# Performance work log

Hardware: AMD Instinct MI355X
Metric: run time of the kernel (lower is better)

## Reference

```python
import jax, jax.numpy as jnp
import numpy as np

H = 16  # n_heads


def setup_inputs() -> dict:
    key = jax.random.key(0)
    ks = jax.random.split(key, 8)
    N, L, dm = 4, 2048, 1024
    scale = 0.02
    rn = lambda k, shape: jax.random.normal(k, shape, dtype=jnp.float32)
    return {
        "queries": rn(ks[0], (N, L, dm)),
        "keys": rn(ks[1], (N, L, dm)),
        "values": rn(ks[2], (N, L, dm)),
        "Wq": rn(ks[3], (dm, dm)) * scale, "bq": jnp.zeros((dm,), jnp.float32),
        "Wk": rn(ks[4], (dm, dm)) * scale, "bk": jnp.zeros((dm,), jnp.float32),
        "Wv": rn(ks[5], (dm, dm)) * scale, "bv": jnp.zeros((dm,), jnp.float32),
        "Wo": rn(ks[6], (dm, dm)) * scale, "bo": jnp.zeros((dm,), jnp.float32),
    }


def _forward(queries, keys, values, Wq, bq, Wk, bk, Wv, bv, Wo, bo):
    N, L, _ = queries.shape
    q = (queries @ Wq + bq).reshape(N, L, H, -1)  # [N,L,H,D]
    k = (keys @ Wk + bk).reshape(N, L, H, -1)     # [N,L,H,D]
    v = (values @ Wv + bv).reshape(N, L, H, -1)   # [N,L,H,K]
    qp = jax.nn.elu(q) + 1.0
    kp = jax.nn.elu(k) + 1.0
    D = qp.shape[-1]
    K = v.shape[-1]

    # Causal linear attention: cumulative outer-product recurrence over time.
    def step(sums, inp):
        q_t, k_t, v_t = inp  # each [N,H,D] / [N,H,K]
        sums = sums + jnp.einsum('bhd,bhk->bhdk', k_t, v_t)
        out_t = jnp.einsum('bhdk,bhd->bhk', sums, q_t)
        return sums, out_t

    init = jnp.zeros((N, H, D, K), qp.dtype)
    xs = (jnp.swapaxes(qp, 0, 1), jnp.swapaxes(kp, 0, 1), jnp.swapaxes(v, 0, 1))
    _, res = jax.lax.scan(step, init, xs)  # [L,N,H,K]
    res = jnp.swapaxes(res, 0, 1)          # [N,L,H,K]
    # Original divides elementwise by cumsum of query features (D == K).
    Z = jnp.cumsum(qp, axis=1)             # [N,L,H,D]
    out = (res / Z).reshape(N, L, -1)
    return out @ Wo + bo


def reference(queries, keys, values, Wq, bq, Wk, bk, Wv, bv, Wo, bo):
    return _forward(queries, keys, values, Wq, bq, Wk, bk, Wv, bv, Wo, bo)
```

## Files before the change

kernel.cpp:

```cpp
#include <hip/hip_runtime.h>
#include <hip/hip_bf16.h>

typedef __hip_bfloat16 bf16;

#define N_B   4
#define LSEQ  2048
#define DM    1024
#define NH    16
#define HD    64
#define MROWS (N_B * LSEQ)
#define TCH   64
#define NC    (LSEQ / TCH)
#define PS    72

typedef short bf16x8 __attribute__((ext_vector_type(8)));
typedef float f32x4  __attribute__((ext_vector_type(4)));

__device__ __forceinline__ float u2f(unsigned short u){ return __uint_as_float(((unsigned)u) << 16); }
__device__ __forceinline__ unsigned short f2u(float x){
    bf16 h = __float2bfloat16(x);
    return *reinterpret_cast<unsigned short*>(&h);
}

__device__ __forceinline__ void g2l16(const void* g, void* l) {
    __builtin_amdgcn_global_load_lds(
        (const __attribute__((address_space(1))) unsigned int*)g,
        (__attribute__((address_space(3))) unsigned int*)l, 16, 0, 0);
}

__global__ __launch_bounds__(256) void cvt_f32_bf16(
    const float* __restrict__ x, bf16* __restrict__ y, int n4)
{
    int i = blockIdx.x * 256 + threadIdx.x;
    if (i < n4) {
        float4 v = ((const float4*)x)[i];
        ushort4 o = make_ushort4(f2u(v.x), f2u(v.y), f2u(v.z), f2u(v.w));
        ((ushort4*)y)[i] = o;
    }
}

__global__ __launch_bounds__(256) void transpose_w(
    const float* __restrict__ W, bf16* __restrict__ Wt)
{
    __shared__ unsigned short t[64][65];
    const int n0 = blockIdx.x * 64;
    const int k0 = blockIdx.y * 64;
    #pragma unroll
    for (int i = 0; i < 16; ++i) {
        int e = i * 256 + threadIdx.x;
        int r = e >> 6, c = e & 63;
        t[c][r] = f2u(W[(size_t)(k0 + r) * DM + n0 + c]);
    }
    __syncthreads();
    #pragma unroll
    for (int i = 0; i < 16; ++i) {
        int e = i * 256 + threadIdx.x;
        int r = e >> 6, c = e & 63;
        ((unsigned short*)Wt)[(size_t)(n0 + r) * DM + k0 + c] = t[r][c];
    }
}

template <int ACT, typename TO>
__global__ __launch_bounds__(256) void gemm_mfma(
    const bf16* __restrict__ A, const bf16* __restrict__ Bt,
    const float* __restrict__ bias, TO* __restrict__ C,
    int M, int N, int K)
{
    __shared__ __align__(16) short As[128 * 32];
    __shared__ __align__(16) short Bs[128 * 32];

    const int tid  = threadIdx.x;
    const int m0   = blockIdx.x * 128;
    const int n0   = blockIdx.y * 128;
    const int wave = tid >> 6;
    const int lane = tid & 63;
    const int wm   = (wave >> 1) * 64;
    const int wn   = (wave & 1) * 64;
    const int quad = lane >> 4;
    const int l16  = lane & 15;

    f32x4 acc[4][4] = {};

    for (int k0 = 0; k0 < K; k0 += 32) {
        #pragma unroll
        for (int i = 0; i < 2; ++i) {
            int e = i * 256 + tid;
            int row = e >> 2, kg = e & 3;
            g2l16(A  + (size_t)(m0 + row) * K + k0 + kg * 8, As + e * 8);
            g2l16(Bt + (size_t)(n0 + row) * K + k0 + kg * 8, Bs + e * 8);
        }
        __syncthreads();

        bf16x8 af[4], bf_[4];
        #pragma unroll
        for (int mi = 0; mi < 4; ++mi)
            af[mi] = *(const bf16x8*)&As[(wm + mi * 16 + l16) * 32 + quad * 8];
        #pragma unroll
        for (int ni = 0; ni < 4; ++ni)
            bf_[ni] = *(const bf16x8*)&Bs[(wn + ni * 16 + l16) * 32 + quad * 8];

        #pragma unroll
        for (int mi = 0; mi < 4; ++mi)
            #pragma unroll
            for (int ni = 0; ni < 4; ++ni)
                acc[mi][ni] = __builtin_amdgcn_mfma_f32_16x16x32_bf16(
                    af[mi], bf_[ni], acc[mi][ni], 0, 0, 0);

        __syncthreads();
    }

    #pragma unroll
    for (int ni = 0; ni < 4; ++ni) {
        int col = n0 + wn + ni * 16 + l16;
        float bv = bias[col];
        #pragma unroll
        for (int mi = 0; mi < 4; ++mi) {
            #pragma unroll
            for (int r = 0; r < 4; ++r) {
                int row = m0 + wm + mi * 16 + quad * 4 + r;
                float x = acc[mi][ni][r] + bv;
                if (ACT) x = (x > 0.f) ? (x + 1.f) : __expf(x);
                if constexpr (sizeof(TO) == 2)
                    ((bf16*)C)[(size_t)row * N + col] = __float2bfloat16(x);
                else
                    ((float*)C)[(size_t)row * N + col] = x;
            }
        }
    }
}

__global__ __launch_bounds__(256) void chunk_state(
    const bf16* __restrict__ qp, const bf16* __restrict__ kp,
    const bf16* __restrict__ v,
    float* __restrict__ chunkS, float* __restrict__ chunkZ)
{
    __shared__ __align__(16) unsigned short kpT_s[64 * PS];
    __shared__ __align__(16) unsigned short vT_s [64 * PS];
    __shared__ __align__(16) unsigned short qp_s [64 * PS];
    __shared__ float red[4][64];

    const int bh = blockIdx.x;
    const int c  = blockIdx.y;
    const int n  = bh >> 4, h = bh & 15;
    const int tid = threadIdx.x;
    const size_t rowbase = (size_t)n * LSEQ + (size_t)c * TCH;

    #pragma unroll
    for (int r = 0; r < 4; ++r) {
        int q = r * 256 + tid;
        int t = q >> 4, c0 = (q & 15) * 4;
        size_t g = (rowbase + t) * DM + h * HD + c0;
        ushort4 ku = *(const ushort4*)((const unsigned short*)kp + g);
        ushort4 vu = *(const ushort4*)((const unsigned short*)v  + g);
        ushort4 qu = *(const ushort4*)((const unsigned short*)qp + g);
        kpT_s[(c0+0)*PS + t] = ku.x;  kpT_s[(c0+1)*PS + t] = ku.y;
        kpT_s[(c0+2)*PS + t] = ku.z;  kpT_s[(c0+3)*PS + t] = ku.w;
        vT_s [(c0+0)*PS + t] = vu.x;  vT_s [(c0+1)*PS + t] = vu.y;
        vT_s [(c0+2)*PS + t] = vu.z;  vT_s [(c0+3)*PS + t] = vu.w;
        *(ushort4*)&qp_s[t * PS + c0] = qu;
    }
    __syncthreads();

    const int wave = tid >> 6, lane = tid & 63;
    const int quad = lane >> 4, l16 = lane & 15;

    f32x4 acc[4] = {};
    #pragma unroll
    for (int kk = 0; kk < 2; ++kk) {
        bf16x8 af = *(const bf16x8*)&kpT_s[(wave*16 + l16) * PS + kk*32 + quad*8];
        #pragma unroll
        for (int ni = 0; ni < 4; ++ni) {
            bf16x8 bfr = *(const bf16x8*)&vT_s[(ni*16 + l16) * PS + kk*32 + quad*8];
            acc[ni] = __builtin_amdgcn_mfma_f32_16x16x32_bf16(af, bfr, acc[ni], 0, 0, 0);
        }
    }
    float* Sout = chunkS + (((size_t)bh * NC + c) << 12);
    #pragma unroll
    for (int ni = 0; ni < 4; ++ni) {
        int k = ni*16 + l16;
        #pragma unroll
        for (int r = 0; r < 4; ++r) {
            int d = wave*16 + quad*4 + r;
            Sout[d * 64 + k] = acc[ni][r];
        }
    }

    {
        int d = tid & 63, part = tid >> 6;
        float s = 0.f;
        #pragma unroll
        for (int t = part*16; t < part*16 + 16; ++t)
            s += u2f(qp_s[t * PS + d]);
        red[part][d] = s;
    }
    __syncthreads();
    if (tid < 64)
        chunkZ[((size_t)bh * NC + c) * 64 + tid] =
            red[0][tid] + red[1][tid] + red[2][tid] + red[3][tid];
}

__global__ __launch_bounds__(256) void prefix_state(
    const float* __restrict__ chunkS, bf16* __restrict__ SpB,
    float* __restrict__ chunkZ)
{
    const int bh = blockIdx.x;
    const int elem = blockIdx.y * 256 + threadIdx.x;
    const float* p = chunkS + (((size_t)bh * NC) << 12) + elem;
    unsigned short* o = (unsigned short*)SpB + (((size_t)bh * NC) << 12) + elem;
    float run = 0.f;
    #pragma unroll
    for (int c = 0; c < NC; ++c) {
        float x = p[(size_t)c << 12];
        o[(size_t)c << 12] = f2u(run);
        run += x;
    }
    if (blockIdx.y == 0 && threadIdx.x < 64) {
        float* pz = chunkZ + (size_t)bh * NC * 64 + threadIdx.x;
        float rz = 0.f;
        for (int c = 0; c < NC; ++c) {
            float x = pz[c * 64];
            pz[c * 64] = rz;
            rz += x;
        }
    }
}

__global__ __launch_bounds__(256) void chunk_attn(
    const bf16* __restrict__ qp, const bf16* __restrict__ kp,
    const bf16* __restrict__ v, const bf16* __restrict__ SpB,
    const float* __restrict__ chunkZ, bf16* __restrict__ att)
{
    __shared__ __align__(16) unsigned short qp_s [64 * PS];
    __shared__ __align__(16) unsigned short kp_s [64 * PS];
    __shared__ __align__(16) unsigned short SpT_s[64 * PS];
    __shared__ __align__(16) unsigned short vT_s [64 * PS];
    __shared__ __align__(16) unsigned short qpT_s[64 * PS];
    __shared__ __align__(16) unsigned short P_s  [64 * PS];

    const int bh = blockIdx.x;
    const int c  = blockIdx.y;
    const int n  = bh >> 4, h = bh & 15;
    const int tid = threadIdx.x;
    const size_t rowbase = (size_t)n * LSEQ + (size_t)c * TCH;
    const unsigned short* Spb = (const unsigned short*)SpB + (((size_t)bh * NC + c) << 12);

    #pragma unroll
    for (int r = 0; r < 4; ++r) {
        int q = r * 256 + tid;
        int t = q >> 4, c0 = (q & 15) * 4;
        size_t g = (rowbase + t) * DM + h * HD + c0;
        ushort4 qu = *(const ushort4*)((const unsigned short*)qp + g);
        ushort4 ku = *(const ushort4*)((const unsigned short*)kp + g);
        ushort4 vu = *(const ushort4*)((const unsigned short*)v  + g);
        ushort4 su = *(const ushort4*)(Spb + q * 4);
        *(ushort4*)&qp_s[t * PS + c0] = qu;
        *(ushort4*)&kp_s[t * PS + c0] = ku;
        vT_s [(c0+0)*PS + t] = vu.x;  vT_s [(c0+1)*PS + t] = vu.y;
        vT_s [(c0+2)*PS + t] = vu.z;  vT_s [(c0+3)*PS + t] = vu.w;
        qpT_s[(c0+0)*PS + t] = qu.x;  qpT_s[(c0+1)*PS + t] = qu.y;
        qpT_s[(c0+2)*PS + t] = qu.z;  qpT_s[(c0+3)*PS + t] = qu.w;
        SpT_s[(c0+0)*PS + t] = su.x;  SpT_s[(c0+1)*PS + t] = su.y;
        SpT_s[(c0+2)*PS + t] = su.z;  SpT_s[(c0+3)*PS + t] = su.w;
    }
    __syncthreads();

    const int wave = tid >> 6, lane = tid & 63;
    const int quad = lane >> 4, l16 = lane & 15;
    const int mrow = wave * 16;

    f32x4 acc[4]  = {};
    f32x4 zacc[4] = {};
    f32x4 pacc[4] = {};

    const unsigned short ONE = 0x3F80;

    #pragma unroll
    for (int kk = 0; kk < 2; ++kk) {
        bf16x8 af = *(const bf16x8*)&qp_s[(mrow + l16) * PS + kk*32 + quad*8];
        bf16x8 tf;
        #pragma unroll
        for (int j = 0; j < 8; ++j) {
            int s = kk*32 + quad*8 + j;
            tf[j] = (short)((s <= mrow + l16) ? ONE : 0);
        }
        #pragma unroll
        for (int ni = 0; ni < 4; ++ni) {
            int boff = (ni*16 + l16) * PS + kk*32 + quad*8;
            bf16x8 b_sp = *(const bf16x8*)&SpT_s[boff];
            bf16x8 b_kp = *(const bf16x8*)&kp_s [boff];
            bf16x8 b_qt = *(const bf16x8*)&qpT_s[boff];
            acc [ni] = __builtin_amdgcn_mfma_f32_16x16x32_bf16(af, b_sp, acc [ni], 0, 0, 0);
            pacc[ni] = __builtin_amdgcn_mfma_f32_16x16x32_bf16(af, b_kp, pacc[ni], 0, 0, 0);
            zacc[ni] = __builtin_amdgcn_mfma_f32_16x16x32_bf16(tf, b_qt, zacc[ni], 0, 0, 0);
        }
    }

    #pragma unroll
    for (int ni = 0; ni < 4; ++ni) {
        int s = ni*16 + l16;
        #pragma unroll
        for (int r = 0; r < 4; ++r) {
            int t = mrow + quad*4 + r;
            float pv = (s <= t) ? pacc[ni][r] : 0.f;
            P_s[t * PS + s] = f2u(pv);
        }
    }
    __syncthreads();

    #pragma unroll
    for (int kk = 0; kk < 2; ++kk) {
        bf16x8 af = *(const bf16x8*)&P_s[(mrow + l16) * PS + kk*32 + quad*8];
        #pragma unroll
        for (int ni = 0; ni < 4; ++ni) {
            bf16x8 b_v = *(const bf16x8*)&vT_s[(ni*16 + l16) * PS + kk*32 + quad*8];
            acc[ni] = __builtin_amdgcn_mfma_f32_16x16x32_bf16(af, b_v, acc[ni], 0, 0, 0);
        }
    }

    #pragma unroll
    for (int ni = 0; ni < 4; ++ni) {
        int k = ni*16 + l16;
        float zp = chunkZ[((size_t)bh * NC + c) * 64 + k];
        #pragma unroll
        for (int r = 0; r < 4; ++r) {
            int t = mrow + quad*4 + r;
            float o = acc[ni][r] / (zp + zacc[ni][r]);
            ((unsigned short*)att)[(rowbase + t) * DM + h * HD + k] = f2u(o);
        }
    }
}

extern "C" void kernel_launch(void* const* d_in, const int* in_sizes, int n_in,
                              void* d_out, int out_size, void* d_ws, size_t ws_size,
                              hipStream_t stream)
{
    const float* queries = (const float*)d_in[0];
    const float* keys    = (const float*)d_in[1];
    const float* values  = (const float*)d_in[2];
    const float* Wq = (const float*)d_in[3];
    const float* bq = (const float*)d_in[4];
    const float* Wk = (const float*)d_in[5];
    const float* bk = (const float*)d_in[6];
    const float* Wv = (const float*)d_in[7];
    const float* bv = (const float*)d_in[8];
    const float* Wo = (const float*)d_in[9];
    const float* bo = (const float*)d_in[10];
    float* out = (float*)d_out;

    char* w = (char*)d_ws;
    const size_t E2 = (size_t)MROWS * DM * 2;
    const size_t WB = (size_t)DM * DM * 2;
    bf16* qb  = (bf16*)(w + 0 * E2);
    bf16* kb  = (bf16*)(w + 1 * E2);
    bf16* vb  = (bf16*)(w + 2 * E2);
    bf16* Wqt = (bf16*)(w + 3 * E2 + 0 * WB);
    bf16* Wkt = (bf16*)(w + 3 * E2 + 1 * WB);
    bf16* Wvt = (bf16*)(w + 3 * E2 + 2 * WB);
    bf16* Wot = (bf16*)(w + 3 * E2 + 3 * WB);
    bf16* qp  = (bf16*)(w + 3 * E2 + 4 * WB);
    bf16* kp  = (bf16*)(w + 4 * E2 + 4 * WB);
    bf16* vv  = (bf16*)(w + 5 * E2 + 4 * WB);
    bf16* SpB = (bf16*)(w + 6 * E2 + 4 * WB);
    float* chunkS = (float*)kb;
    float* chunkZ = (float*)Wqt;
    bf16*  att    = qb;

    const int n4 = (MROWS * DM) / 4;
    cvt_f32_bf16<<<n4 / 256, 256, 0, stream>>>(queries, qb, n4);
    cvt_f32_bf16<<<n4 / 256, 256, 0, stream>>>(keys,    kb, n4);
    cvt_f32_bf16<<<n4 / 256, 256, 0, stream>>>(values,  vb, n4);

    dim3 tgrid(DM / 64, DM / 64);
    transpose_w<<<tgrid, 256, 0, stream>>>(Wq, Wqt);
    transpose_w<<<tgrid, 256, 0, stream>>>(Wk, Wkt);
    transpose_w<<<tgrid, 256, 0, stream>>>(Wv, Wvt);
    transpose_w<<<tgrid, 256, 0, stream>>>(Wo, Wot);

    dim3 ggrid(MROWS / 128, DM / 128);
    gemm_mfma<1, bf16><<<ggrid, 256, 0, stream>>>(qb, Wqt, bq, qp, MROWS, DM, DM);
    gemm_mfma<1, bf16><<<ggrid, 256, 0, stream>>>(kb, Wkt, bk, kp, MROWS, DM, DM);
    gemm_mfma<0, bf16><<<ggrid, 256, 0, stream>>>(vb, Wvt, bv, vv, MROWS, DM, DM);

    chunk_state <<<dim3(64, NC), 256, 0, stream>>>(qp, kp, vv, chunkS, chunkZ);
    prefix_state<<<dim3(64, 16), 256, 0, stream>>>(chunkS, SpB, chunkZ);
    chunk_attn  <<<dim3(64, NC), 256, 0, stream>>>(qp, kp, vv, SpB, chunkZ, att);

    gemm_mfma<0, float><<<ggrid, 256, 0, stream>>>(att, Wot, bo, out, MROWS, DM, DM);
}
```

Measured before the change: 344.2 us.

## Batch conversion, transpose and projection launches; swizzle GEMM LDS; bf16 chunk states

```diff
diff --git a/kernel.cpp b/kernel.cpp
--- a/kernel.cpp
+++ b/kernel.cpp
@@ -28,20 +28,29 @@
         (__attribute__((address_space(3))) unsigned int*)l, 16, 0, 0);
 }
 
-__global__ __launch_bounds__(256) void cvt_f32_bf16(
-    const float* __restrict__ x, bf16* __restrict__ y, int n4)
-{
-    int i = blockIdx.x * 256 + threadIdx.x;
-    if (i < n4) {
-        float4 v = ((const float4*)x)[i];
-        ushort4 o = make_ushort4(f2u(v.x), f2u(v.y), f2u(v.z), f2u(v.w));
-        ((ushort4*)y)[i] = o;
-    }
-}
-
-__global__ __launch_bounds__(256) void transpose_w(
-    const float* __restrict__ W, bf16* __restrict__ Wt)
-{
+__global__ __launch_bounds__(256) void cvt3_f32_bf16(
+    const float* __restrict__ x0, const float* __restrict__ x1, const float* __restrict__ x2,
+    bf16* __restrict__ y0, bf16* __restrict__ y1, bf16* __restrict__ y2, int per)
+{
+    int which = blockIdx.x / per;
+    const float* x = (which == 0) ? x0 : (which == 1) ? x1 : x2;
+    bf16* y = (which == 0) ? y0 : (which == 1) ? y1 : y2;
+    int i = (blockIdx.x - which * per) * 256 + threadIdx.x;
+    float4 v = ((const float4*)x)[i];
+    ushort4 o = make_ushort4(f2u(v.x), f2u(v.y), f2u(v.z), f2u(v.w));
+    ((ushort4*)y)[i] = o;
+}
+
+__global__ __launch_bounds__(256) void transpose_w4(
+    const float* __restrict__ W0, const float* __restrict__ W1,
+    const float* __restrict__ W2, const float* __restrict__ W3,
+    bf16* __restrict__ T0, bf16* __restrict__ T1,
+    bf16* __restrict__ T2, bf16* __restrict__ T3)
+{
+    const int z = blockIdx.z;
+    const float* W = (z == 0) ? W0 : (z == 1) ? W1 : (z == 2) ? W2 : W3;
+    bf16* Wt = (z == 0) ? T0 : (z == 1) ? T1 : (z == 2) ? T2 : T3;
+
     __shared__ unsigned short t[64][65];
     const int n0 = blockIdx.x * 64;
     const int k0 = blockIdx.y * 64;
@@ -60,12 +69,21 @@
     }
 }
 
-template <int ACT, typename TO>
-__global__ __launch_bounds__(256) void gemm_mfma(
-    const bf16* __restrict__ A, const bf16* __restrict__ Bt,
-    const float* __restrict__ bias, TO* __restrict__ C,
-    int M, int N, int K)
-{
+template <typename TO>
+__global__ __launch_bounds__(256) void gemm_mfma3(
+    const bf16* __restrict__ A0, const bf16* __restrict__ A1, const bf16* __restrict__ A2,
+    const bf16* __restrict__ B0, const bf16* __restrict__ B1, const bf16* __restrict__ B2,
+    const float* __restrict__ c0, const float* __restrict__ c1, const float* __restrict__ c2,
+    TO* __restrict__ C0, TO* __restrict__ C1, TO* __restrict__ C2,
+    int actMask, int M, int N, int K)
+{
+    const int z = blockIdx.z;
+    const bf16* A  = (z == 0) ? A0 : (z == 1) ? A1 : A2;
+    const bf16* Bt = (z == 0) ? B0 : (z == 1) ? B1 : B2;
+    const float* bias = (z == 0) ? c0 : (z == 1) ? c1 : c2;
+    TO* C = (z == 0) ? C0 : (z == 1) ? C1 : C2;
+    const int act = (actMask >> z) & 1;
+
     __shared__ __align__(16) short As[128 * 32];
     __shared__ __align__(16) short Bs[128 * 32];
 
@@ -78,26 +96,28 @@
     const int wn   = (wave & 1) * 64;
     const int quad = lane >> 4;
     const int l16  = lane & 15;
+    const int ksw  = (quad ^ (l16 & 3)) * 8;
 
     f32x4 acc[4][4] = {};
 
-    for (int k0 = 0; k0 < K; k0 += 32) {
+    for (int k0i = 0; k0i < K; k0i += 32) {
         #pragma unroll
         for (int i = 0; i < 2; ++i) {
             int e = i * 256 + tid;
             int row = e >> 2, kg = e & 3;
-            g2l16(A  + (size_t)(m0 + row) * K + k0 + kg * 8, As + e * 8);
-            g2l16(Bt + (size_t)(n0 + row) * K + k0 + kg * 8, Bs + e * 8);
+            int kgs = (kg ^ (row & 3)) * 8;
+            g2l16(A  + (size_t)(m0 + row) * K + k0i + kgs, As + e * 8);
+            g2l16(Bt + (size_t)(n0 + row) * K + k0i + kgs, Bs + e * 8);
         }
         __syncthreads();
 
         bf16x8 af[4], bf_[4];
         #pragma unroll
         for (int mi = 0; mi < 4; ++mi)
-            af[mi] = *(const bf16x8*)&As[(wm + mi * 16 + l16) * 32 + quad * 8];
+            af[mi] = *(const bf16x8*)&As[(wm + mi * 16 + l16) * 32 + ksw];
         #pragma unroll
         for (int ni = 0; ni < 4; ++ni)
-            bf_[ni] = *(const bf16x8*)&Bs[(wn + ni * 16 + l16) * 32 + quad * 8];
+            bf_[ni] = *(const bf16x8*)&Bs[(wn + ni * 16 + l16) * 32 + ksw];
 
         #pragma unroll
         for (int mi = 0; mi < 4; ++mi)
@@ -119,7 +139,7 @@
             for (int r = 0; r < 4; ++r) {
                 int row = m0 + wm + mi * 16 + quad * 4 + r;
                 float x = acc[mi][ni][r] + bv;
-                if (ACT) x = (x > 0.f) ? (x + 1.f) : __expf(x);
+                if (act) x = (x > 0.f) ? (x + 1.f) : __expf(x);
                 if constexpr (sizeof(TO) == 2)
                     ((bf16*)C)[(size_t)row * N + col] = __float2bfloat16(x);
                 else
@@ -132,7 +152,7 @@
 __global__ __launch_bounds__(256) void chunk_state(
     const bf16* __restrict__ qp, const bf16* __restrict__ kp,
     const bf16* __restrict__ v,
-    float* __restrict__ chunkS, float* __restrict__ chunkZ)
+    bf16* __restrict__ chunkSB, float* __restrict__ chunkZ)
 {
     __shared__ __align__(16) unsigned short kpT_s[64 * PS];
     __shared__ __align__(16) unsigned short vT_s [64 * PS];
@@ -174,14 +194,14 @@
             acc[ni] = __builtin_amdgcn_mfma_f32_16x16x32_bf16(af, bfr, acc[ni], 0, 0, 0);
         }
     }
-    float* Sout = chunkS + (((size_t)bh * NC + c) << 12);
+    unsigned short* Sout = (unsigned short*)chunkSB + (((size_t)bh * NC + c) << 12);
     #pragma unroll
     for (int ni = 0; ni < 4; ++ni) {
         int k = ni*16 + l16;
         #pragma unroll
         for (int r = 0; r < 4; ++r) {
             int d = wave*16 + quad*4 + r;
-            Sout[d * 64 + k] = acc[ni][r];
+            Sout[d * 64 + k] = f2u(acc[ni][r]);
         }
     }
 
@@ -200,17 +220,17 @@
 }
 
 __global__ __launch_bounds__(256) void prefix_state(
-    const float* __restrict__ chunkS, bf16* __restrict__ SpB,
+    const bf16* __restrict__ chunkSB, bf16* __restrict__ SpB,
     float* __restrict__ chunkZ)
 {
     const int bh = blockIdx.x;
     const int elem = blockIdx.y * 256 + threadIdx.x;
-    const float* p = chunkS + (((size_t)bh * NC) << 12) + elem;
+    const unsigned short* p = (const unsigned short*)chunkSB + (((size_t)bh * NC) << 12) + elem;
     unsigned short* o = (unsigned short*)SpB + (((size_t)bh * NC) << 12) + elem;
     float run = 0.f;
     #pragma unroll
     for (int c = 0; c < NC; ++c) {
-        float x = p[(size_t)c << 12];
+        float x = u2f(p[(size_t)c << 12]);
         o[(size_t)c << 12] = f2u(run);
         run += x;
     }
@@ -361,29 +381,26 @@
     bf16* kp  = (bf16*)(w + 4 * E2 + 4 * WB);
     bf16* vv  = (bf16*)(w + 5 * E2 + 4 * WB);
     bf16* SpB = (bf16*)(w + 6 * E2 + 4 * WB);
-    float* chunkS = (float*)kb;
-    float* chunkZ = (float*)Wqt;
-    bf16*  att    = qb;
+    bf16*  chunkSB = kb;
+    float* chunkZ  = (float*)Wqt;
+    bf16*  att     = qb;
 
     const int n4 = (MROWS * DM) / 4;
-    cvt_f32_bf16<<<n4 / 256, 256, 0, stream>>>(queries, qb, n4);
-    cvt_f32_bf16<<<n4 / 256, 256, 0, stream>>>(keys,    kb, n4);
-    cvt_f32_bf16<<<n4 / 256, 256, 0, stream>>>(values,  vb, n4);
-
-    dim3 tgrid(DM / 64, DM / 64);
-    transpose_w<<<tgrid, 256, 0, stream>>>(Wq, Wqt);
-    transpose_w<<<tgrid, 256, 0, stream>>>(Wk, Wkt);
-    transpose_w<<<tgrid, 256, 0, stream>>>(Wv, Wvt);
-    transpose_w<<<tgrid, 256, 0, stream>>>(Wo, Wot);
-
-    dim3 ggrid(MROWS / 128, DM / 128);
-    gemm_mfma<1, bf16><<<ggrid, 256, 0, stream>>>(qb, Wqt, bq, qp, MROWS, DM, DM);
-    gemm_mfma<1, bf16><<<ggrid, 256, 0, stream>>>(kb, Wkt, bk, kp, MROWS, DM, DM);
-    gemm_mfma<0, bf16><<<ggrid, 256, 0, stream>>>(vb, Wvt, bv, vv, MROWS, DM, DM);
-
-    chunk_state <<<dim3(64, NC), 256, 0, stream>>>(qp, kp, vv, chunkS, chunkZ);
-    prefix_state<<<dim3(64, 16), 256, 0, stream>>>(chunkS, SpB, chunkZ);
+    const int per = n4 / 256;
+    cvt3_f32_bf16<<<3 * per, 256, 0, stream>>>(queries, keys, values, qb, kb, vb, per);
+
+    transpose_w4<<<dim3(DM / 64, DM / 64, 4), 256, 0, stream>>>(
+        Wq, Wk, Wv, Wo, Wqt, Wkt, Wvt, Wot);
+
+    gemm_mfma3<bf16><<<dim3(MROWS / 128, DM / 128, 3), 256, 0, stream>>>(
+        qb, kb, vb, Wqt, Wkt, Wvt, bq, bk, bv, qp, kp, vv,
+        0b011, MROWS, DM, DM);
+
+    chunk_state <<<dim3(64, NC), 256, 0, stream>>>(qp, kp, vv, chunkSB, chunkZ);
+    prefix_state<<<dim3(64, 16), 256, 0, stream>>>(chunkSB, SpB, chunkZ);
     chunk_attn  <<<dim3(64, NC), 256, 0, stream>>>(qp, kp, vv, SpB, chunkZ, att);
 
-    gemm_mfma<0, float><<<ggrid, 256, 0, stream>>>(att, Wot, bo, out, MROWS, DM, DM);
-}
+    gemm_mfma3<float><<<dim3(MROWS / 128, DM / 128, 1), 256, 0, stream>>>(
+        att, att, att, Wot, Wot, Wot, bo, bo, bo, out, out, out,
+        0, MROWS, DM, DM);
+}
```

Measured after the change: 310.6 us. 9.8% less time.
